# Optimization experiments

Measured on AMD Instinct MI355X. Metric: run time of the kernel, lower is better.

## Reference

```python
import jax, jax.numpy as jnp
import numpy as np

B, L, P, T, D, H = 16, 50, 49, 20, 512, 8
DH = D // H
DFF = 4 * D
EPS = 1e-6
NEG = -1000000000.0


def gelu_tanh(x):
    return 0.5 * x * (1.0 + jnp.tanh(jnp.sqrt(2.0 / jnp.pi) * (x + 0.044715 * x ** 3)))


def layernorm(x, a, b):
    # torch LayerNorm (custom): unbiased std, divide by (std + eps)
    mean = jnp.mean(x, axis=-1, keepdims=True)
    std = jnp.sqrt(jnp.var(x, axis=-1, keepdims=True, ddof=1))
    return a * (x - mean) / (std + EPS) + b


def setup_inputs() -> dict:
    key = jax.random.key(0)
    ks = jax.random.split(key, 20)
    s = 0.02
    return {
        "img": jax.random.normal(ks[0], (B, L, P, D), jnp.float32),
        "title": jax.random.normal(ks[1], (B, L, T, D), jnp.float32),
        "mask": jax.random.randint(ks[2], (B, L, T), 0, 2, jnp.int32),
        "scale_img": jax.random.normal(ks[3], (H, P), jnp.float32) * 0.1,
        "scale_title": jax.random.normal(ks[4], (H, T), jnp.float32) * 0.1,
        "w_proj": jax.random.normal(ks[5], (D, D), jnp.float32) * s,
        "b_proj": jnp.zeros((D,), jnp.float32),
        "w1_img": jax.random.normal(ks[6], (DFF, D), jnp.float32) * s,
        "b1_img": jnp.zeros((DFF,), jnp.float32),
        "w2_img": jax.random.normal(ks[7], (D, DFF), jnp.float32) * s,
        "b2_img": jnp.zeros((D,), jnp.float32),
        "w1_tit": jax.random.normal(ks[8], (DFF, D), jnp.float32) * s,
        "b1_tit": jnp.zeros((DFF,), jnp.float32),
        "w2_tit": jax.random.normal(ks[9], (D, DFF), jnp.float32) * s,
        "b2_tit": jnp.zeros((D,), jnp.float32),
        "ln_a_img": jnp.ones((D,), jnp.float32),
        "ln_b_img": jnp.zeros((D,), jnp.float32),
        "ln_a_tit": jnp.ones((D,), jnp.float32),
        "ln_b_tit": jnp.zeros((D,), jnp.float32),
    }


def _forward(img, title, mask, scale_img, scale_title, w_proj, b_proj,
             w1_img, b1_img, w2_img, b2_img, w1_tit, b1_tit, w2_tit, b2_tit,
             ln_a_img, ln_b_img, ln_a_tit, ln_b_tit):
    imgh = img.reshape(B, L, P, H, DH)      # [B,L,P,H,dh]
    tith = title.reshape(B, L, T, H, DH)    # [B,L,T,H,dh]

    raw = jnp.einsum('blphd,blthd->blhpt', imgh, tith) / jnp.sqrt(jnp.float32(DH))
    # corr_title is the transpose of the UNSCALED corr_img
    corr_img = raw * scale_img[None, None, :, :, None]                     # [B,L,H,P,T]
    corr_tit = jnp.swapaxes(raw, -1, -2) * scale_title[None, None, :, :, None]  # [B,L,H,T,P]

    m_img = mask[:, :, None, None, :]  # [B,L,1,1,T] -> broadcast over H,P
    m_tit = mask[:, :, None, :, None]  # [B,L,1,T,1]
    corr_img = jnp.where(m_img == 0, NEG, corr_img)
    corr_tit = jnp.where(m_tit == 0, NEG, corr_tit)

    p_img = jax.nn.softmax(corr_img, axis=-1)  # [B,L,H,P,T]
    p_tit = jax.nn.softmax(corr_tit, axis=-1)  # [B,L,H,T,P]

    # T != P, so the torch code takes the else branch (swapped outputs)
    hid_img = jnp.einsum('blhtp,blphd->blthd', p_tit, imgh).reshape(B, L, T, D)
    hid_tit = jnp.einsum('blhpt,blthd->blphd', p_img, tith).reshape(B, L, P, D)

    # both projected with img_layer (faithful to source)
    hid_img = hid_img @ w_proj.T + b_proj
    hid_tit = hid_tit @ w_proj.T + b_proj

    ffn_img = gelu_tanh(hid_img @ w1_img.T + b1_img) @ w2_img.T + b2_img
    ffn_tit = gelu_tanh(hid_tit @ w1_tit.T + b1_tit) @ w2_tit.T + b2_tit

    out_img = hid_img + layernorm(ffn_img, ln_a_img, ln_b_img)
    out_tit = hid_tit + layernorm(ffn_tit, ln_a_tit, ln_b_tit)
    return out_img, out_tit


def reference(img, title, mask, scale_img, scale_title, w_proj, b_proj,
              w1_img, b1_img, w2_img, b2_img, w1_tit, b1_tit, w2_tit, b2_tit,
              ln_a_img, ln_b_img, ln_a_tit, ln_b_tit):
    return _forward(img, title, mask, scale_img, scale_title, w_proj, b_proj,
                    w1_img, b1_img, w2_img, b2_img, w1_tit, b1_tit, w2_tit, b2_tit,
                    ln_a_img, ln_b_img, ln_a_tit, ln_b_tit)
```

## Files before the change

kernel.cpp:

```cpp
#include <hip/hip_runtime.h>
#include <hip/hip_bf16.h>

#define BB   16
#define LL   50
#define PP   49
#define TT   20
#define DD   512
#define HH   8
#define DHH  64
#define DFF  2048

#define BL     (BB*LL)
#define ROWS_I (BL*TT)
#define ROWS_T (BL*PP)
#define ROWS_A (ROWS_I+ROWS_T)
#define OUT_I_ELEMS ((size_t)ROWS_I*DD)
#define CHUNK 19600

#define R1_OFF 80281600ull
#define R2_OFF 136806400ull
#define R3_OFF 176947200ull

typedef __attribute__((ext_vector_type(8))) short bf16x8;
typedef __attribute__((ext_vector_type(4))) float f32x4;

__device__ __forceinline__ unsigned short f2bf(float f) {
    union { float f; unsigned int i; } w; w.f = f;
    unsigned int x = w.i;
    unsigned int r = (x + 0x7fffu + ((x >> 16) & 1u)) >> 16;
    return (unsigned short)r;
}
__device__ __forceinline__ float gelu_fast(float x) {
    float c2 = 1.5957691216057308f * (x + 0.044715f * x * x * x);
    return x / (1.0f + __expf(-c2));
}

__global__ __launch_bounds__(256) void cvt_kernel(
    const float* __restrict__ s, unsigned short* __restrict__ d, int n4)
{
    int i = blockIdx.x * 256 + threadIdx.x;
    if (i < n4) {
        float4 v = ((const float4*)s)[i];
        ushort4 u;
        u.x = f2bf(v.x); u.y = f2bf(v.y); u.z = f2bf(v.z); u.w = f2bf(v.w);
        ((ushort4*)d)[i] = u;
    }
}

__global__ __launch_bounds__(256) void attn_kernel(
    const float* __restrict__ img, const float* __restrict__ title,
    const int* __restrict__ mask, const float* __restrict__ scale_img,
    const float* __restrict__ scale_tit, unsigned short* __restrict__ hid)
{
    const int blh = blockIdx.x;
    const int h  = blh & 7;
    const int bl = blh >> 3;
    const int tid = threadIdx.x;
    const int wave = tid >> 6;
    const int lane = tid & 63;

    __shared__ __align__(16) float simg[PP][68];
    __shared__ __align__(16) float stit[TT][68];
    __shared__ __align__(16) float S [PP][TT];
    __shared__ __align__(16) float pI[PP][TT];
    __shared__ __align__(16) float pT[TT][52];
    __shared__ int   msk[TT];

    const float* imgbase = img   + (size_t)bl * PP * DD + h * DHH;
    const float* titbase = title + (size_t)bl * TT * DD + h * DHH;

    for (int i = tid; i < PP * 16; i += 256) {
        int p = i >> 4, d4 = i & 15;
        *(float4*)&simg[p][d4 * 4] = *(const float4*)(imgbase + (size_t)p * DD + d4 * 4);
    }
    for (int i = tid; i < TT * 16; i += 256) {
        int t = i >> 4, d4 = i & 15;
        *(float4*)&stit[t][d4 * 4] = *(const float4*)(titbase + (size_t)t * DD + d4 * 4);
    }
    if (tid < TT) msk[tid] = mask[bl * TT + tid];
    __syncthreads();

    if (tid < PP * 5) {
        const int p  = tid / 5;
        const int tg = tid - p * 5;
        float a0 = 0.f, a1 = 0.f, a2 = 0.f, a3 = 0.f;
        #pragma unroll 4
        for (int d = 0; d < DHH; d += 4) {
            float4 a  = *(const float4*)&simg[p][d];
            float4 b0 = *(const float4*)&stit[tg     ][d];
            float4 b1 = *(const float4*)&stit[tg +  5][d];
            float4 b2 = *(const float4*)&stit[tg + 10][d];
            float4 b3 = *(const float4*)&stit[tg + 15][d];
            a0 += a.x*b0.x + a.y*b0.y + a.z*b0.z + a.w*b0.w;
            a1 += a.x*b1.x + a.y*b1.y + a.z*b1.z + a.w*b1.w;
            a2 += a.x*b2.x + a.y*b2.y + a.z*b2.z + a.w*b2.w;
            a3 += a.x*b3.x + a.y*b3.y + a.z*b3.z + a.w*b3.w;
        }
        S[p][tg     ] = a0 * 0.125f;
        S[p][tg +  5] = a1 * 0.125f;
        S[p][tg + 10] = a2 * 0.125f;
        S[p][tg + 15] = a3 * 0.125f;
    }
    __syncthreads();

    if (tid < PP) {
        const int p = tid;
        const float sc = scale_img[h * PP + p];
        float m = -1e30f;
        #pragma unroll
        for (int t = 0; t < TT; ++t) {
            float x = (msk[t] == 0) ? -1e9f : S[p][t] * sc;
            m = fmaxf(m, x);
        }
        float sum = 0.f;
        #pragma unroll
        for (int t = 0; t < TT; ++t) {
            float x = (msk[t] == 0) ? -1e9f : S[p][t] * sc;
            float e = __expf(x - m);
            pI[p][t] = e; sum += e;
        }
        float inv = 1.f / sum;
        #pragma unroll
        for (int t = 0; t < TT; ++t) pI[p][t] *= inv;
    }
    if (tid >= 64 && tid < 64 + TT) {
        const int t = tid - 64;
        const float sc = scale_tit[h * TT + t];
        const bool dead = (msk[t] == 0);
        float m = -1e30f;
        #pragma unroll
        for (int p = 0; p < PP; ++p) {
            float x = dead ? -1e9f : S[p][t] * sc;
            m = fmaxf(m, x);
        }
        float sum = 0.f;
        #pragma unroll
        for (int p = 0; p < PP; ++p) {
            float x = dead ? -1e9f : S[p][t] * sc;
            float e = __expf(x - m);
            pT[t][p] = e; sum += e;
        }
        float inv = 1.f / sum;
        #pragma unroll
        for (int p = 0; p < PP; ++p) pT[t][p] *= inv;
    }
    __syncthreads();

    {
        float accA[5] = {0.f, 0.f, 0.f, 0.f, 0.f};
        #pragma unroll
        for (int p = 0; p < 48; p += 4) {
            float v0 = simg[p + 0][lane];
            float v1 = simg[p + 1][lane];
            float v2 = simg[p + 2][lane];
            float v3 = simg[p + 3][lane];
            #pragma unroll
            for (int j = 0; j < 5; ++j) {
                const int t = wave + j * 4;
                float4 w4 = *(const float4*)&pT[t][p];
                accA[j] += v0 * w4.x + v1 * w4.y + v2 * w4.z + v3 * w4.w;
            }
        }
        {
            float v0 = simg[48][lane];
            #pragma unroll
            for (int j = 0; j < 5; ++j)
                accA[j] += v0 * pT[wave + j * 4][48];
        }
        #pragma unroll
        for (int j = 0; j < 5; ++j) {
            const int t = wave + j * 4;
            hid[(size_t)(bl * TT + t) * DD + h * DHH + lane] = f2bf(accA[j]);
        }
    }

    {
        float accB[13] = {0.f,0.f,0.f,0.f,0.f,0.f,0.f,0.f,0.f,0.f,0.f,0.f,0.f};
        #pragma unroll
        for (int t = 0; t < TT; t += 4) {
            float v0 = stit[t + 0][lane];
            float v1 = stit[t + 1][lane];
            float v2 = stit[t + 2][lane];
            float v3 = stit[t + 3][lane];
            #pragma unroll
            for (int j = 0; j < 13; ++j) {
                const int p = wave + j * 4;
                if (p < PP) {
                    float4 w4 = *(const float4*)&pI[p][t];
                    accB[j] += v0 * w4.x + v1 * w4.y + v2 * w4.z + v3 * w4.w;
                }
            }
        }
        #pragma unroll
        for (int j = 0; j < 13; ++j) {
            const int p = wave + j * 4;
            if (p < PP)
                hid[OUT_I_ELEMS + (size_t)(bl * PP + p) * DD + h * DHH + lane] = f2bf(accB[j]);
        }
    }
}

template<bool GELU, bool F32OUT, bool BF16OUT>
__global__ __launch_bounds__(256) void gemm_mfma(
    const unsigned short* __restrict__ A, const unsigned short* __restrict__ Bw,
    const float* __restrict__ bias,
    float* __restrict__ Cf, unsigned short* __restrict__ Cb,
    int M, int N, int K)
{
    __shared__ unsigned short As[2][128 * 32];
    __shared__ unsigned short Bs[2][128 * 32];
    const int tid  = threadIdx.x;
    const int wave = tid >> 6;
    const int lane = tid & 63;
    const int row0 = blockIdx.y * 128;
    const int col0 = blockIdx.x * 128;
    const int m_off = (wave >> 1) * 64;
    const int n_off = (wave & 1) * 64;
    const int lane_m = lane & 15;

    const int slot8 = (((lane >> 4) ^ ((lane_m >> 1) & 3)) * 8);

    const int li0 = tid, li1 = 256 + tid;
    const int r0 = li0 >> 2, r1 = li1 >> 2;
    const int c80 = (li0 & 3) ^ ((r0 >> 1) & 3);
    const int c81 = (li1 & 3) ^ ((r1 >> 1) & 3);
    int grA0 = row0 + r0; if (grA0 >= M) grA0 = M - 1;
    int grA1 = row0 + r1; if (grA1 >= M) grA1 = M - 1;
    const unsigned short* aP0 = A  + (size_t)grA0 * K + c80 * 8;
    const unsigned short* aP1 = A  + (size_t)grA1 * K + c81 * 8;
    const unsigned short* bP0 = Bw + (size_t)(col0 + r0) * K + c80 * 8;
    const unsigned short* bP1 = Bw + (size_t)(col0 + r1) * K + c81 * 8;

    f32x4 acc[4][4] = {};

    #define STAGE(buf, k0)                                                          \
        do {                                                                        \
            __builtin_amdgcn_global_load_lds(                                       \
                (const __attribute__((address_space(1))) unsigned int*)(aP0 + (k0)),\
                (__attribute__((address_space(3))) unsigned int*)&As[buf][li0 * 8], \
                16, 0, 0);                                                          \
            __builtin_amdgcn_global_load_lds(                                       \
                (const __attribute__((address_space(1))) unsigned int*)(aP1 + (k0)),\
                (__attribute__((address_space(3))) unsigned int*)&As[buf][li1 * 8], \
                16, 0, 0);                                                          \
            __builtin_amdgcn_global_load_lds(                                       \
                (const __attribute__((address_space(1))) unsigned int*)(bP0 + (k0)),\
                (__attribute__((address_space(3))) unsigned int*)&Bs[buf][li0 * 8], \
                16, 0, 0);                                                          \
            __builtin_amdgcn_global_load_lds(                                       \
                (const __attribute__((address_space(1))) unsigned int*)(bP1 + (k0)),\
                (__attribute__((address_space(3))) unsigned int*)&Bs[buf][li1 * 8], \
                16, 0, 0);                                                          \
        } while (0)

    STAGE(0, 0);
    __syncthreads();

    const int nk = K >> 5;
    for (int t = 0; t < nk; ++t) {
        const int cur = t & 1;
        if (t + 1 < nk) STAGE(cur ^ 1, (t + 1) * 32);

        bf16x8 af[4], bfr[4];
        #pragma unroll
        for (int i = 0; i < 4; ++i) {
            af[i]  = *(const bf16x8*)&As[cur][(m_off + i * 16 + lane_m) * 32 + slot8];
            bfr[i] = *(const bf16x8*)&Bs[cur][(n_off + i * 16 + lane_m) * 32 + slot8];
        }
        #pragma unroll
        for (int i = 0; i < 4; ++i)
            #pragma unroll
            for (int j = 0; j < 4; ++j)
                acc[i][j] = __builtin_amdgcn_mfma_f32_16x16x32_bf16(af[i], bfr[j], acc[i][j], 0, 0, 0);

        __syncthreads();
    }
    #undef STAGE

    #pragma unroll
    for (int i = 0; i < 4; ++i) {
        #pragma unroll
        for (int r = 0; r < 4; ++r) {
            const int row = row0 + m_off + i * 16 + (lane >> 4) * 4 + r;
            if (row < M) {
                #pragma unroll
                for (int j = 0; j < 4; ++j) {
                    const int col = col0 + n_off + j * 16 + lane_m;
                    float v = acc[i][j][r] + bias[col];
                    if (GELU) v = gelu_fast(v);
                    if (F32OUT)  Cf[(size_t)row * N + col] = v;
                    if (BF16OUT) Cb[(size_t)row * N + col] = f2bf(v);
                }
            }
        }
    }
}

__global__ __launch_bounds__(256) void ln_res_kernel(
    const float* __restrict__ f2, float* __restrict__ out,
    const float* __restrict__ a, const float* __restrict__ b, int M)
{
    const int wave = threadIdx.x >> 6;
    const int lane = threadIdx.x & 63;
    const int row = blockIdx.x * 4 + wave;
    if (row >= M) return;
    const float* x = f2 + (size_t)row * DD;
    float* o = out + (size_t)row * DD;

    float xs[8];
    float s1 = 0.f, s2 = 0.f;
    #pragma unroll
    for (int i = 0; i < 8; ++i) {
        float v = x[lane + i * 64];
        xs[i] = v; s1 += v; s2 += v * v;
    }
    #pragma unroll
    for (int off = 32; off > 0; off >>= 1) {
        s1 += __shfl_xor(s1, off, 64);
        s2 += __shfl_xor(s2, off, 64);
    }
    const float mean = s1 * (1.f / 512.f);
    float var = (s2 - 512.f * mean * mean) * (1.f / 511.f);
    var = fmaxf(var, 0.f);
    const float rinv = 1.f / (sqrtf(var) + 1e-6f);
    #pragma unroll
    for (int i = 0; i < 8; ++i) {
        const int d = lane + i * 64;
        o[d] = o[d] + a[d] * (xs[i] - mean) * rinv + b[d];
    }
}

extern "C" void kernel_launch(void* const* d_in, const int* in_sizes, int n_in,
                              void* d_out, int out_size, void* d_ws, size_t ws_size,
                              hipStream_t stream) {
    const float* img       = (const float*)d_in[0];
    const float* title     = (const float*)d_in[1];
    const int*   mask      = (const int*)  d_in[2];
    const float* scale_img = (const float*)d_in[3];
    const float* scale_tit = (const float*)d_in[4];
    const float* w_proj    = (const float*)d_in[5];
    const float* b_proj    = (const float*)d_in[6];
    const float* w1_img    = (const float*)d_in[7];
    const float* b1_img    = (const float*)d_in[8];
    const float* w2_img    = (const float*)d_in[9];
    const float* b2_img    = (const float*)d_in[10];
    const float* w1_tit    = (const float*)d_in[11];
    const float* b1_tit    = (const float*)d_in[12];
    const float* w2_tit    = (const float*)d_in[13];
    const float* b2_tit    = (const float*)d_in[14];
    const float* ln_a_img  = (const float*)d_in[15];
    const float* ln_b_img  = (const float*)d_in[16];
    const float* ln_a_tit  = (const float*)d_in[17];
    const float* ln_b_tit  = (const float*)d_in[18];

    float* out = (float*)d_out;
    unsigned short* hid_bf = (unsigned short*)d_ws;
    unsigned short* act    = (unsigned short*)d_ws;
    unsigned short* out_bf = (unsigned short*)((char*)d_ws + R1_OFF);
    float*          f2     = (float*)((char*)d_ws + R2_OFF);
    unsigned short* wp_bf  = (unsigned short*)((char*)d_ws + R3_OFF);
    unsigned short* w1i_bf = wp_bf  + 262144;
    unsigned short* w2i_bf = w1i_bf + 1048576;
    unsigned short* w1t_bf = w2i_bf + 1048576;
    unsigned short* w2t_bf = w1t_bf + 1048576;

    cvt_kernel<<<(262144/4 + 255)/256, 256, 0, stream>>>(w_proj, wp_bf, 262144/4);
    cvt_kernel<<<(1048576/4 + 255)/256, 256, 0, stream>>>(w1_img, w1i_bf, 1048576/4);
    cvt_kernel<<<(1048576/4 + 255)/256, 256, 0, stream>>>(w2_img, w2i_bf, 1048576/4);
    cvt_kernel<<<(1048576/4 + 255)/256, 256, 0, stream>>>(w1_tit, w1t_bf, 1048576/4);
    cvt_kernel<<<(1048576/4 + 255)/256, 256, 0, stream>>>(w2_tit, w2t_bf, 1048576/4);

    attn_kernel<<<BL * HH, 256, 0, stream>>>(img, title, mask, scale_img, scale_tit, hid_bf);

    gemm_mfma<false, true, true><<<dim3(DD/128, (ROWS_A + 127)/128), 256, 0, stream>>>(
        hid_bf, wp_bf, b_proj, out, out_bf, ROWS_A, DD, DD);

    gemm_mfma<true, false, true><<<dim3(DFF/128, (ROWS_I + 127)/128), 256, 0, stream>>>(
        out_bf, w1i_bf, b1_img, nullptr, act, ROWS_I, DFF, DD);
    gemm_mfma<false, true, false><<<dim3(DD/128, (ROWS_I + 127)/128), 256, 0, stream>>>(
        act, w2i_bf, b2_img, f2, nullptr, ROWS_I, DD, DFF);
    ln_res_kernel<<<(ROWS_I + 3)/4, 256, 0, stream>>>(f2, out, ln_a_img, ln_b_img, ROWS_I);

    for (int c = 0; c < 2; ++c) {
        const unsigned short* a1 = out_bf + (size_t)(ROWS_I + c * CHUNK) * DD;
        float* o1 = out + OUT_I_ELEMS + (size_t)c * CHUNK * DD;
        gemm_mfma<true, false, true><<<dim3(DFF/128, (CHUNK + 127)/128), 256, 0, stream>>>(
            a1, w1t_bf, b1_tit, nullptr, act, CHUNK, DFF, DD);
        gemm_mfma<false, true, false><<<dim3(DD/128, (CHUNK + 127)/128), 256, 0, stream>>>(
            act, w2t_bf, b2_tit, f2, nullptr, CHUNK, DD, DFF);
        ln_res_kernel<<<(CHUNK + 3)/4, 256, 0, stream>>>(f2, o1, ln_a_tit, ln_b_tit, CHUNK);
    }
}
```

Before: 828.7 us.

## Fuse second FFN GEMM with bias, layernorm and residual in one kernel

Replaces the second FFN GEMM plus a separate layernorm/residual kernel with a single kernel. Each 512-thread block computes a 64-row by full-512-column tile, reduces row statistics across waves through shared memory, and applies layernorm and the residual add in the epilogue. This removes the f32 intermediate write and re-read and one launch per call. The cost is a tall-skinny tile with a 64KB B buffer, a grid of only a few hundred blocks, and less A-tile reuse. It also changes the LDS swizzle pattern in the generic GEMM.

After: 891.1 us. +7.5%, slower.

```diff
diff --git a/kernel.cpp b/kernel.cpp
--- a/kernel.cpp
+++ b/kernel.cpp
@@ -218,12 +218,12 @@
     const int n_off = (wave & 1) * 64;
     const int lane_m = lane & 15;
 
-    const int slot8 = (((lane >> 4) ^ ((lane_m >> 1) & 3)) * 8);
+    const int slot8 = (((lane >> 4) ^ (lane_m & 3)) * 8);
 
     const int li0 = tid, li1 = 256 + tid;
     const int r0 = li0 >> 2, r1 = li1 >> 2;
-    const int c80 = (li0 & 3) ^ ((r0 >> 1) & 3);
-    const int c81 = (li1 & 3) ^ ((r1 >> 1) & 3);
+    const int c80 = (li0 & 3) ^ (r0 & 3);
+    const int c81 = (li1 & 3) ^ (r1 & 3);
     int grA0 = row0 + r0; if (grA0 >= M) grA0 = M - 1;
     int grA1 = row0 + r1; if (grA1 >= M) grA1 = M - 1;
     const unsigned short* aP0 = A  + (size_t)grA0 * K + c80 * 8;
@@ -296,37 +296,126 @@
     }
 }
 
-__global__ __launch_bounds__(256) void ln_res_kernel(
-    const float* __restrict__ f2, float* __restrict__ out,
-    const float* __restrict__ a, const float* __restrict__ b, int M)
+__global__ __launch_bounds__(512) void ffn2_ln_kernel(
+    const unsigned short* __restrict__ act2, const unsigned short* __restrict__ W2,
+    const float* __restrict__ b2, const float* __restrict__ lna,
+    const float* __restrict__ lnb, float* __restrict__ out, int M)
 {
-    const int wave = threadIdx.x >> 6;
-    const int lane = threadIdx.x & 63;
-    const int row = blockIdx.x * 4 + wave;
-    if (row >= M) return;
-    const float* x = f2 + (size_t)row * DD;
-    float* o = out + (size_t)row * DD;
-
-    float xs[8];
-    float s1 = 0.f, s2 = 0.f;
+    __shared__ unsigned short As[2][64 * 32];
+    __shared__ unsigned short Bs[2][512 * 32];
+    __shared__ float red[64][8][2];
+
+    const int tid  = threadIdx.x;
+    const int wn   = tid >> 6;
+    const int lane = tid & 63;
+    const int lm   = lane & 15;
+    const int kg   = lane >> 4;
+    const int s8   = (kg ^ (lm & 3)) * 8;
+    const int row0 = blockIdx.x * 64;
+
+    const int sr = tid >> 2;
+    const int c8 = ((tid & 3) ^ (sr & 3)) * 8;
+    int ar = row0 + sr; if (ar >= M) ar = M - 1;
+    const unsigned short* aP = act2 + (size_t)ar * DFF + c8;
+    const unsigned short* bP[4];
     #pragma unroll
-    for (int i = 0; i < 8; ++i) {
-        float v = x[lane + i * 64];
-        xs[i] = v; s1 += v; s2 += v * v;
-    }
+    for (int q = 0; q < 4; ++q)
+        bP[q] = W2 + (size_t)(q * 128 + sr) * DFF + c8;
+
+    #define STAGE2(buf, t)                                                           \
+        do {                                                                         \
+            const int ko_ = (t) * 32;                                                \
+            if (tid < 256)                                                           \
+                __builtin_amdgcn_global_load_lds(                                    \
+                    (const __attribute__((address_space(1))) unsigned int*)(aP + ko_), \
+                    (__attribute__((address_space(3))) unsigned int*)&As[buf][tid * 8], \
+                    16, 0, 0);                                                       \
+            _Pragma("unroll")                                                        \
+            for (int q_ = 0; q_ < 4; ++q_)                                           \
+                __builtin_amdgcn_global_load_lds(                                    \
+                    (const __attribute__((address_space(1))) unsigned int*)(bP[q_] + ko_), \
+                    (__attribute__((address_space(3))) unsigned int*)&Bs[buf][(q_ * 512 + tid) * 8], \
+                    16, 0, 0);                                                       \
+        } while (0)
+
+    f32x4 acc[4][4] = {};
+
+    STAGE2(0, 0);
+    __syncthreads();
+
+    const int nt = DFF >> 5;
+    for (int t = 0; t < nt; ++t) {
+        const int cur = t & 1;
+        if (t + 1 < nt) STAGE2(cur ^ 1, t + 1);
+
+        bf16x8 af[4], bfr[4];
+        #pragma unroll
+        for (int i = 0; i < 4; ++i)
+            af[i] = *(const bf16x8*)&As[cur][(i * 16 + lm) * 32 + s8];
+        #pragma unroll
+        for (int j = 0; j < 4; ++j)
+            bfr[j] = *(const bf16x8*)&Bs[cur][(wn * 64 + j * 16 + lm) * 32 + s8];
+        #pragma unroll
+        for (int i = 0; i < 4; ++i)
+            #pragma unroll
+            for (int j = 0; j < 4; ++j)
+                acc[i][j] = __builtin_amdgcn_mfma_f32_16x16x32_bf16(af[i], bfr[j], acc[i][j], 0, 0, 0);
+
+        __syncthreads();
+    }
+    #undef STAGE2
+
+    float bv[4];
     #pragma unroll
-    for (int off = 32; off > 0; off >>= 1) {
-        s1 += __shfl_xor(s1, off, 64);
-        s2 += __shfl_xor(s2, off, 64);
-    }
-    const float mean = s1 * (1.f / 512.f);
-    float var = (s2 - 512.f * mean * mean) * (1.f / 511.f);
-    var = fmaxf(var, 0.f);
-    const float rinv = 1.f / (sqrtf(var) + 1e-6f);
+    for (int j = 0; j < 4; ++j) bv[j] = b2[wn * 64 + j * 16 + lm];
+
     #pragma unroll
-    for (int i = 0; i < 8; ++i) {
-        const int d = lane + i * 64;
-        o[d] = o[d] + a[d] * (xs[i] - mean) * rinv + b[d];
+    for (int i = 0; i < 4; ++i) {
+        #pragma unroll
+        for (int r = 0; r < 4; ++r) {
+            float s1 = 0.f, s2 = 0.f;
+            #pragma unroll
+            for (int j = 0; j < 4; ++j) {
+                float v = acc[i][j][r] + bv[j];
+                acc[i][j][r] = v;
+                s1 += v; s2 += v * v;
+            }
+            #pragma unroll
+            for (int off = 8; off > 0; off >>= 1) {
+                s1 += __shfl_xor(s1, off, 64);
+                s2 += __shfl_xor(s2, off, 64);
+            }
+            if (lm == 0) {
+                const int lrow = i * 16 + kg * 4 + r;
+                red[lrow][wn][0] = s1;
+                red[lrow][wn][1] = s2;
+            }
+        }
+    }
+    __syncthreads();
+
+    #pragma unroll
+    for (int i = 0; i < 4; ++i) {
+        #pragma unroll
+        for (int r = 0; r < 4; ++r) {
+            const int lrow = i * 16 + kg * 4 + r;
+            const int grow = row0 + lrow;
+            float S1 = 0.f, S2 = 0.f;
+            #pragma unroll
+            for (int w = 0; w < 8; ++w) { S1 += red[lrow][w][0]; S2 += red[lrow][w][1]; }
+            const float mean = S1 * (1.f / 512.f);
+            float var = (S2 - 512.f * mean * mean) * (1.f / 511.f);
+            var = fmaxf(var, 0.f);
+            const float rinv = 1.f / (sqrtf(var) + 1e-6f);
+            if (grow < M) {
+                #pragma unroll
+                for (int j = 0; j < 4; ++j) {
+                    const int col = wn * 64 + j * 16 + lm;
+                    float* op = out + (size_t)grow * DD + col;
+                    *op = *op + lna[col] * (acc[i][j][r] - mean) * rinv + lnb[col];
+                }
+            }
+        }
     }
 }
 
@@ -357,7 +446,6 @@
     unsigned short* hid_bf = (unsigned short*)d_ws;
     unsigned short* act    = (unsigned short*)d_ws;
     unsigned short* out_bf = (unsigned short*)((char*)d_ws + R1_OFF);
-    float*          f2     = (float*)((char*)d_ws + R2_OFF);
     unsigned short* wp_bf  = (unsigned short*)((char*)d_ws + R3_OFF);
     unsigned short* w1i_bf = wp_bf  + 262144;
     unsigned short* w2i_bf = w1i_bf + 1048576;
@@ -377,17 +465,15 @@
 
     gemm_mfma<true, false, true><<<dim3(DFF/128, (ROWS_I + 127)/128), 256, 0, stream>>>(
         out_bf, w1i_bf, b1_img, nullptr, act, ROWS_I, DFF, DD);
-    gemm_mfma<false, true, false><<<dim3(DD/128, (ROWS_I + 127)/128), 256, 0, stream>>>(
-        act, w2i_bf, b2_img, f2, nullptr, ROWS_I, DD, DFF);
-    ln_res_kernel<<<(ROWS_I + 3)/4, 256, 0, stream>>>(f2, out, ln_a_img, ln_b_img, ROWS_I);
+    ffn2_ln_kernel<<<(ROWS_I + 63)/64, 512, 0, stream>>>(
+        act, w2i_bf, b2_img, ln_a_img, ln_b_img, out, ROWS_I);
 
     for (int c = 0; c < 2; ++c) {
         const unsigned short* a1 = out_bf + (size_t)(ROWS_I + c * CHUNK) * DD;
         float* o1 = out + OUT_I_ELEMS + (size_t)c * CHUNK * DD;
         gemm_mfma<true, false, true><<<dim3(DFF/128, (CHUNK + 127)/128), 256, 0, stream>>>(
             a1, w1t_bf, b1_tit, nullptr, act, CHUNK, DFF, DD);
-        gemm_mfma<false, true, false><<<dim3(DD/128, (CHUNK + 127)/128), 256, 0, stream>>>(
-            act, w2t_bf, b2_tit, f2, nullptr, CHUNK, DD, DFF);
-        ln_res_kernel<<<(CHUNK + 3)/4, 256, 0, stream>>>(f2, o1, ln_a_tit, ln_b_tit, CHUNK);
-    }
-}
+        ffn2_ln_kernel<<<(CHUNK + 63)/64, 512, 0, stream>>>(
+            act, w2t_bf, b2_tit, ln_a_tit, ln_b_tit, o1, CHUNK);
+    }
+}
```

## Add 256x256-tile 4-stage pipelined GEMM for projection and FFN-up layers

Applied to the files above, without the earlier changes.

Adds a new MFMA GEMM kernel with 256x256 output tiles, 512 threads (8 waves, each computing a 128x64 sub-tile), and a 4-buffer LDS ring filled by direct global-to-LDS loads with explicit vmcnt waits and raised priority around the MFMA block. It is used for the projection GEMM and the first FFN GEMM (with GELU) of both branches, while the K=2048 down-projection stays on the old 128x128 kernel. The larger tile raises data reuse per LDS load and cuts global traffic. In exchange it uses 128 KB of LDS and many accumulator registers, which limits occupancy, and it launches fewer blocks, so the last wave of blocks may leave CUs idle.

Measured after the change: 880.7 us. 6.3% more time.

```diff
diff --git a/kernel.cpp b/kernel.cpp
--- a/kernel.cpp
+++ b/kernel.cpp
@@ -287,6 +287,117 @@
                 for (int j = 0; j < 4; ++j) {
                     const int col = col0 + n_off + j * 16 + lane_m;
                     float v = acc[i][j][r] + bias[col];
+                    if (GELU) v = gelu_fast(v);
+                    if (F32OUT)  Cf[(size_t)row * N + col] = v;
+                    if (BF16OUT) Cb[(size_t)row * N + col] = f2bf(v);
+                }
+            }
+        }
+    }
+}
+
+template<bool GELU, bool F32OUT, bool BF16OUT>
+__global__ __launch_bounds__(512) void gemm_256(
+    const unsigned short* __restrict__ A, const unsigned short* __restrict__ Bw,
+    const float* __restrict__ bias,
+    float* __restrict__ Cf, unsigned short* __restrict__ Cb,
+    int M, int N, int K)
+{
+    __shared__ unsigned short As[4][256 * 32];
+    __shared__ unsigned short Bs[4][256 * 32];
+
+    const int tid  = threadIdx.x;
+    const int wid  = tid >> 6;
+    const int lane = tid & 63;
+    const int wm   = wid >> 2;
+    const int wn   = wid & 3;
+    const int row0 = blockIdx.y * 256;
+    const int col0 = blockIdx.x * 256;
+    const int lm   = lane & 15;
+    const int kg   = lane >> 4;
+    const int s8   = (kg ^ ((lm >> 1) & 3)) * 8;
+
+    const int sr = tid >> 2;
+    const int g8 = ((tid & 3) ^ ((tid >> 3) & 3)) * 8;
+    const unsigned short* aP[2];
+    const unsigned short* bP[2];
+    #pragma unroll
+    for (int q = 0; q < 2; ++q) {
+        int ar = row0 + q * 128 + sr; if (ar >= M) ar = M - 1;
+        aP[q] = A  + (size_t)ar * K + g8;
+        bP[q] = Bw + (size_t)(col0 + q * 128 + sr) * K + g8;
+    }
+
+    #define STAGE6(buf, kt)                                                          \
+        do {                                                                         \
+            const int ko_ = (kt) * 32;                                               \
+            _Pragma("unroll")                                                        \
+            for (int q_ = 0; q_ < 2; ++q_) {                                         \
+                __builtin_amdgcn_global_load_lds(                                    \
+                    (const __attribute__((address_space(1))) unsigned int*)(aP[q_] + ko_), \
+                    (__attribute__((address_space(3))) unsigned int*)&As[buf][(q_ * 512 + tid) * 8], \
+                    16, 0, 0);                                                       \
+                __builtin_amdgcn_global_load_lds(                                    \
+                    (const __attribute__((address_space(1))) unsigned int*)(bP[q_] + ko_), \
+                    (__attribute__((address_space(3))) unsigned int*)&Bs[buf][(q_ * 512 + tid) * 8], \
+                    16, 0, 0);                                                       \
+            }                                                                        \
+        } while (0)
+
+    f32x4 acc[8][4] = {};
+
+    const int nkt = K >> 5;
+    STAGE6(0, 0);
+    STAGE6(1, 1);
+    STAGE6(2, 2);
+
+    for (int p = 0; p < nkt; ++p) {
+        const int b = p & 3;
+        const int rem = nkt - 1 - p;
+        if (rem >= 2)      asm volatile("s_waitcnt vmcnt(8)" ::: "memory");
+        else if (rem == 1) asm volatile("s_waitcnt vmcnt(4)" ::: "memory");
+        else               asm volatile("s_waitcnt vmcnt(0)" ::: "memory");
+        __builtin_amdgcn_s_barrier();
+        asm volatile("" ::: "memory");
+
+        if (p + 3 < nkt) STAGE6((p + 3) & 3, p + 3);
+
+        const unsigned short* Ab = &As[b][0];
+        const unsigned short* Bb = &Bs[b][0];
+        bf16x8 af[8], bfr[4];
+        #pragma unroll
+        for (int i = 0; i < 8; ++i)
+            af[i] = *(const bf16x8*)&Ab[(wm * 128 + i * 16 + lm) * 32 + s8];
+        #pragma unroll
+        for (int j = 0; j < 4; ++j)
+            bfr[j] = *(const bf16x8*)&Bb[(wn * 64 + j * 16 + lm) * 32 + s8];
+
+        __builtin_amdgcn_s_setprio(1);
+        #pragma unroll
+        for (int i = 0; i < 8; ++i)
+            #pragma unroll
+            for (int j = 0; j < 4; ++j)
+                acc[i][j] = __builtin_amdgcn_mfma_f32_16x16x32_bf16(af[i], bfr[j], acc[i][j], 0, 0, 0);
+        __builtin_amdgcn_s_setprio(0);
+        asm volatile("" ::: "memory");
+    }
+    #undef STAGE6
+
+    float bv[4];
+    #pragma unroll
+    for (int n = 0; n < 4; ++n) bv[n] = bias[col0 + wn * 64 + n * 16 + lm];
+
+    const int orow0 = row0 + wm * 128 + (lane >> 4) * 4;
+    #pragma unroll
+    for (int m = 0; m < 8; ++m) {
+        #pragma unroll
+        for (int r = 0; r < 4; ++r) {
+            const int row = orow0 + m * 16 + r;
+            if (row < M) {
+                #pragma unroll
+                for (int n = 0; n < 4; ++n) {
+                    const int col = col0 + wn * 64 + n * 16 + lm;
+                    float v = acc[m][n][r] + bv[n];
                     if (GELU) v = gelu_fast(v);
                     if (F32OUT)  Cf[(size_t)row * N + col] = v;
                     if (BF16OUT) Cb[(size_t)row * N + col] = f2bf(v);
@@ -372,10 +483,10 @@
 
     attn_kernel<<<BL * HH, 256, 0, stream>>>(img, title, mask, scale_img, scale_tit, hid_bf);
 
-    gemm_mfma<false, true, true><<<dim3(DD/128, (ROWS_A + 127)/128), 256, 0, stream>>>(
+    gemm_256<false, true, true><<<dim3(DD/256, (ROWS_A + 255)/256), 512, 0, stream>>>(
         hid_bf, wp_bf, b_proj, out, out_bf, ROWS_A, DD, DD);
 
-    gemm_mfma<true, false, true><<<dim3(DFF/128, (ROWS_I + 127)/128), 256, 0, stream>>>(
+    gemm_256<true, false, true><<<dim3(DFF/256, (ROWS_I + 255)/256), 512, 0, stream>>>(
         out_bf, w1i_bf, b1_img, nullptr, act, ROWS_I, DFF, DD);
     gemm_mfma<false, true, false><<<dim3(DD/128, (ROWS_I + 127)/128), 256, 0, stream>>>(
         act, w2i_bf, b2_img, f2, nullptr, ROWS_I, DD, DFF);
@@ -384,7 +495,7 @@
     for (int c = 0; c < 2; ++c) {
         const unsigned short* a1 = out_bf + (size_t)(ROWS_I + c * CHUNK) * DD;
         float* o1 = out + OUT_I_ELEMS + (size_t)c * CHUNK * DD;
-        gemm_mfma<true, false, true><<<dim3(DFF/128, (CHUNK + 127)/128), 256, 0, stream>>>(
+        gemm_256<true, false, true><<<dim3(DFF/256, (CHUNK + 255)/256), 512, 0, stream>>>(
             a1, w1t_bf, b1_tit, nullptr, act, CHUNK, DFF, DD);
         gemm_mfma<false, true, false><<<dim3(DD/128, (CHUNK + 127)/128), 256, 0, stream>>>(
             act, w2t_bf, b2_tit, f2, nullptr, CHUNK, DD, DFF);
```
